# Performance work log

Hardware: AMD Instinct MI355X
Metric: run time of the kernel (lower is better)

The kernel has to match this reference:

```python
import jax, jax.numpy as jnp
import numpy as np


def setup_inputs() -> dict:
    key = jax.random.key(0)
    k1, k2, k3 = jax.random.split(key, 3)
    S, G, B, C, P = 3, 8, 2048, 512, 64
    node_feats = jax.random.normal(k1, (S, G * B, C), dtype=jnp.float32)
    weight = jax.random.normal(k2, (P, C), dtype=jnp.float32)
    smooth_factor = jax.random.normal(k3, (P,), dtype=jnp.float32)
    return {
        "node_feats": node_feats,
        "weight": weight,
        "smooth_factor": smooth_factor,
        "batch_size": B,
        "num_graphs": G,
    }


def reference(node_feats, weight, smooth_factor, batch_size, num_graphs):
    # node_feats: [S, N_scale, C] (scales stacked; torch version takes a list and cats)
    S, Ns, C = node_feats.shape
    P = weight.shape[0]
    x = node_feats.reshape(-1, C)                       # [N, C], N = S*Ns

    # RBF-style score: (2*c.x - |x|^2 - |c|^2), clamped at 0, scaled by beta
    cx = x @ weight.T                                   # [N, P]
    x_sq = jnp.sum(x * x, axis=1, keepdims=True)        # [N, 1]
    c_sq = jnp.sum(weight * weight, axis=1)[None, :]    # [1, P]
    beta = jax.nn.sigmoid(smooth_factor)                # [P]
    logits = jnp.minimum(2.0 * cx - x_sq - c_sq, 0.0) / beta[None, :]
    assign = jax.nn.softmax(logits, axis=1)             # [N, P]

    # Per-graph weighted sum (uniform batch_list), accumulated across scales:
    # out[g] = sum_{s,n in graph g} assign[s,g,n]^T feats[s,g,n]
    a = assign.reshape(S, num_graphs, batch_size, P)
    f = node_feats.reshape(S, num_graphs, batch_size, C)
    outputs = jnp.einsum('sgnp,sgnc->gpc', a, f)        # [G, P, C]
    return outputs, assign
```

## Files before the change

kernel.cpp:

```cpp
#include <hip/hip_runtime.h>
#include <math.h>

#define S_ 3
#define G_ 8
#define B_ 2048
#define C_ 512
#define P_ 64
#define N_ (S_ * G_ * B_)

typedef __attribute__((ext_vector_type(8))) short short8;
typedef __attribute__((ext_vector_type(4))) float f32x4;
typedef __attribute__((ext_vector_type(4))) unsigned int uint4v;

__device__ __forceinline__ unsigned f2bf1(float f) {
    union { float f; unsigned u; } c; c.f = f;
    unsigned u = c.u;
    u += 0x7fffu + ((u >> 16) & 1u);
    return u >> 16;
}
__device__ __forceinline__ unsigned pk2(float a, float b) {
    return f2bf1(a) | (f2bf1(b) << 16);
}
__device__ __forceinline__ void gl_lds16(const void* g, void* l) {
    __builtin_amdgcn_global_load_lds(
        (const __attribute__((address_space(1))) void*)g,
        (__attribute__((address_space(3))) void*)l, 16, 0, 0);
}
#define WAIT6_BARRIER() asm volatile("s_waitcnt vmcnt(6)\n\ts_barrier" ::: "memory")
#define WAIT0_BARRIER() asm volatile("s_waitcnt vmcnt(0)\n\ts_barrier" ::: "memory")
#define RAW_BARRIER()   asm volatile("s_barrier" ::: "memory")

__global__ __launch_bounds__(64) void prep_kernel(
    const float* __restrict__ w, const float* __restrict__ sf,
    unsigned short* __restrict__ wb, float* __restrict__ csq,
    float* __restrict__ rbeta)
{
    const int p = blockIdx.x, l = threadIdx.x;
    const float* wr = w + (size_t)p * C_ + l * 8;
    f32x4 a = *(const f32x4*)wr;
    f32x4 b = *(const f32x4*)(wr + 4);
    float s = a[0]*a[0] + a[1]*a[1] + a[2]*a[2] + a[3]*a[3]
            + b[0]*b[0] + b[1]*b[1] + b[2]*b[2] + b[3]*b[3];
    uint4v pk;
    pk.x = pk2(a[0], a[1]); pk.y = pk2(a[2], a[3]);
    pk.z = pk2(b[0], b[1]); pk.w = pk2(b[2], b[3]);
    *(uint4v*)&wb[(size_t)p * C_ + l * 8] = pk;
#pragma unroll
    for (int off = 1; off < 64; off <<= 1) s += __shfl_xor(s, off, 64);
    if (l == 0) csq[p] = s;
    if (p == 0) rbeta[l] = 1.0f + expf(-sf[l]);
}

__global__ __launch_bounds__(256, 3) void assign_v7(
    const float* __restrict__ x, const unsigned short* __restrict__ wb,
    const float* __restrict__ csq, const float* __restrict__ rbeta,
    float* __restrict__ assign, unsigned short* __restrict__ a_t)
{
    __shared__ __align__(16) float xsb[2][64 * 64];
    __shared__ __align__(16) unsigned short wsb[2][64 * 64];
    __shared__ float xsq_s[64];
    float* lg = &xsb[0][0];

    const int t = threadIdx.x, lane = t & 63, wv = t >> 6;
    const int q = lane >> 4, col = lane & 15;
    const int n0 = blockIdx.x * 64;

    const float* gx[4];
#pragma unroll
    for (int i = 0; i < 4; ++i) {
        const int row = 16 * wv + 4 * i + (lane >> 4);
        const int pr  = ((row >> 1) & 7) | (row & 8);
        gx[i] = x + (size_t)(n0 + row) * C_ + (((lane & 15) ^ pr) << 2);
    }
    const unsigned short* gw[2];
#pragma unroll
    for (int i = 0; i < 2; ++i) {
        const int p = 16 * wv + 8 * i + (lane >> 3);
        gw[i] = wb + (size_t)p * C_ + (((lane & 7) ^ (p & 7)) * 8);
    }
    const int prA = ((col >> 1) & 7) | (col & 8);
    const int wg  = col & 7;

    float csqv[4], rbv[4];
#pragma unroll
    for (int nt = 0; nt < 4; ++nt) {
        csqv[nt] = csq[16 * nt + col];
        rbv[nt]  = rbeta[16 * nt + col];
    }

    f32x4 acc[4];
#pragma unroll
    for (int nt = 0; nt < 4; ++nt) acc[nt] = (f32x4){0.f, 0.f, 0.f, 0.f};
    float xsq = 0.f;

#pragma unroll
    for (int i = 0; i < 4; ++i) gl_lds16(gx[i], &xsb[0][(16 * wv + 4 * i) * 64]);
#pragma unroll
    for (int i = 0; i < 2; ++i) gl_lds16(gw[i], &wsb[0][(16 * wv + 8 * i) * 64]);

#pragma unroll
    for (int ch = 0; ch < 8; ++ch) {
        const int cur = ch & 1;
        if (ch < 7) {
            const int k0 = (ch + 1) * 64;
#pragma unroll
            for (int i = 0; i < 4; ++i)
                gl_lds16(gx[i] + k0, &xsb[cur ^ 1][(16 * wv + 4 * i) * 64]);
#pragma unroll
            for (int i = 0; i < 2; ++i)
                gl_lds16(gw[i] + k0, &wsb[cur ^ 1][(16 * wv + 8 * i) * 64]);
            WAIT6_BARRIER();
        } else {
            WAIT0_BARRIER();
        }
#pragma unroll
        for (int s = 0; s < 2; ++s) {
            const int g0 = 8 * s + 2 * q;
            f32x4 f0 = *(const f32x4*)&xsb[cur][(16 * wv + col) * 64 + ((g0 ^ prA) << 2)];
            f32x4 f1 = *(const f32x4*)&xsb[cur][(16 * wv + col) * 64 + (((g0 + 1) ^ prA) << 2)];
            xsq += f0.x*f0.x + f0.y*f0.y + f0.z*f0.z + f0.w*f0.w
                 + f1.x*f1.x + f1.y*f1.y + f1.z*f1.z + f1.w*f1.w;
            union { uint4v u; short8 s8; } cv;
            cv.u.x = pk2(f0.x, f0.y); cv.u.y = pk2(f0.z, f0.w);
            cv.u.z = pk2(f1.x, f1.y); cv.u.w = pk2(f1.z, f1.w);
            const int wgr = 4 * s + q;
#pragma unroll
            for (int nt = 0; nt < 4; ++nt) {
                short8 bf = *(const short8*)&wsb[cur][(16 * nt + col) * 64 + ((wgr ^ wg) * 8)];
                acc[nt] = __builtin_amdgcn_mfma_f32_16x16x32_bf16(cv.s8, bf, acc[nt], 0, 0, 0);
            }
        }
        RAW_BARRIER();
    }

    xsq += __shfl_xor(xsq, 16, 64);
    xsq += __shfl_xor(xsq, 32, 64);
    if (q == 0) xsq_s[16 * wv + col] = xsq;
    __syncthreads();

    float vals[4][4];
#pragma unroll
    for (int reg = 0; reg < 4; ++reg) {
        const int row = 16 * wv + 4 * q + reg;
        const float xq = xsq_s[row];
        float vmax = -3.4e38f;
#pragma unroll
        for (int nt = 0; nt < 4; ++nt) {
            float v = 2.0f * acc[nt][reg] - xq - csqv[nt];
            v = fminf(v, 0.0f) * rbv[nt];
            vals[reg][nt] = v;
            vmax = fmaxf(vmax, v);
        }
#pragma unroll
        for (int off = 1; off < 16; off <<= 1)
            vmax = fmaxf(vmax, __shfl_xor(vmax, off, 64));
        float ss = 0.f;
#pragma unroll
        for (int nt = 0; nt < 4; ++nt) { vals[reg][nt] = __expf(vals[reg][nt] - vmax); ss += vals[reg][nt]; }
#pragma unroll
        for (int off = 1; off < 16; off <<= 1)
            ss += __shfl_xor(ss, off, 64);
        const float inv = 1.0f / ss;
#pragma unroll
        for (int nt = 0; nt < 4; ++nt) vals[reg][nt] *= inv;
    }

#pragma unroll
    for (int reg = 0; reg < 4; ++reg) {
        const int row = 16 * wv + 4 * q + reg;
#pragma unroll
        for (int nt = 0; nt < 4; ++nt)
            lg[row * 68 + 16 * nt + col] = vals[reg][nt];
    }
    __syncthreads();

#pragma unroll
    for (int i = 0; i < 4; ++i) {
        const int f = i * 256 + t;
        const int row = f >> 4, sp = (f & 15) * 4;
        *(f32x4*)(assign + (size_t)(n0 + row) * P_ + sp) = *(const f32x4*)&lg[row * 68 + sp];
    }

    const int p = lane;
    float v[16];
#pragma unroll
    for (int i = 0; i < 16; ++i) v[i] = lg[(wv * 16 + i) * 68 + p];
    uint4v d0, d1;
    d0.x = pk2(v[0], v[1]);   d0.y = pk2(v[2], v[3]);
    d0.z = pk2(v[4], v[5]);   d0.w = pk2(v[6], v[7]);
    d1.x = pk2(v[8], v[9]);   d1.y = pk2(v[10], v[11]);
    d1.z = pk2(v[12], v[13]); d1.w = pk2(v[14], v[15]);
    unsigned short* dst = a_t + (size_t)p * N_ + n0 + wv * 16;
    *(uint4v*)dst = d0;
    *(uint4v*)(dst + 8) = d1;
}

__global__ __launch_bounds__(256, 3) void group_v7(
    const float* __restrict__ x, const unsigned short* __restrict__ a_t,
    float* __restrict__ part)
{
    __shared__ __align__(16) float xsb[2][64 * 64];
    __shared__ __align__(16) unsigned short asb[2][64 * 64];

    const int t = threadIdx.x, lane = t & 63, wv = t >> 6;
    const int q = lane >> 4, col = lane & 15;
    const int g = blockIdx.x, ct = blockIdx.y, ks = blockIdx.z;
    const int c0 = ct * 64, sc = ks >> 2, b0 = (ks & 3) * 512;
    const size_t base = (size_t)sc * (G_ * B_) + (size_t)g * B_ + b0;

    const float* gx[4];
#pragma unroll
    for (int i = 0; i < 4; ++i) {
        const int n  = 16 * wv + 4 * i + (lane >> 4);
        const int pm = ((n >> 3) & 3) | (((n >> 3) & 1) << 2);
        gx[i] = x + (base + n) * C_ + c0 + (((lane & 15) ^ pm) << 2);
    }
    const unsigned short* ga[2];
#pragma unroll
    for (int i = 0; i < 2; ++i) {
        const int p = 16 * wv + 8 * i + (lane >> 3);
        ga[i] = a_t + (size_t)p * N_ + base + (((lane & 7) ^ (p & 7)) * 8);
    }
    const int cl = 16 * wv + col;
    const int permq = q | ((q & 1) << 2);
    const int cswz  = (((cl >> 2) ^ permq) << 2) | (cl & 3);
    const int ag    = col & 7;

    f32x4 acc[4];
#pragma unroll
    for (int mt = 0; mt < 4; ++mt) acc[mt] = (f32x4){0.f, 0.f, 0.f, 0.f};

#pragma unroll
    for (int i = 0; i < 4; ++i) gl_lds16(gx[i], &xsb[0][(16 * wv + 4 * i) * 64]);
#pragma unroll
    for (int i = 0; i < 2; ++i) gl_lds16(ga[i], &asb[0][(16 * wv + 8 * i) * 64]);

#pragma unroll
    for (int ch = 0; ch < 8; ++ch) {
        const int cur = ch & 1;
        if (ch < 7) {
            const int nb = (ch + 1) * 64;
#pragma unroll
            for (int i = 0; i < 4; ++i)
                gl_lds16(gx[i] + (size_t)nb * C_, &xsb[cur ^ 1][(16 * wv + 4 * i) * 64]);
#pragma unroll
            for (int i = 0; i < 2; ++i)
                gl_lds16(ga[i] + nb, &asb[cur ^ 1][(16 * wv + 8 * i) * 64]);
            WAIT6_BARRIER();
        } else {
            WAIT0_BARRIER();
        }
#pragma unroll
        for (int s = 0; s < 2; ++s) {
            const int koff = s * 32 + q * 8;
            float gv[8];
#pragma unroll
            for (int j = 0; j < 8; ++j) gv[j] = xsb[cur][(koff + j) * 64 + cswz];
            union { uint4v u; short8 s8; } cv;
            cv.u.x = pk2(gv[0], gv[1]); cv.u.y = pk2(gv[2], gv[3]);
            cv.u.z = pk2(gv[4], gv[5]); cv.u.w = pk2(gv[6], gv[7]);
            const int agr = 4 * s + q;
#pragma unroll
            for (int mt = 0; mt < 4; ++mt) {
                short8 af = *(const short8*)&asb[cur][(16 * mt + col) * 64 + ((agr ^ ag) * 8)];
                acc[mt] = __builtin_amdgcn_mfma_f32_16x16x32_bf16(af, cv.s8, acc[mt], 0, 0, 0);
            }
        }
        RAW_BARRIER();
    }

    float* pt = part + (((size_t)(g * 8 + ct) * 12) + ks) * 4096;
#pragma unroll
    for (int mt = 0; mt < 4; ++mt)
#pragma unroll
        for (int reg = 0; reg < 4; ++reg) {
            const int p = 16 * mt + 4 * q + reg;
            pt[p * 64 + cl] = acc[mt][reg];
        }
}

__global__ __launch_bounds__(256) void reduce_out(
    const float* __restrict__ part, float* __restrict__ out)
{
    const int idx = blockIdx.x * 256 + threadIdx.x;
    const int g = idx >> 15, r = idx & 32767;
    const int p = r >> 9,  c = r & 511;
    const int ct = c >> 6, cl = c & 63;
    const float* src = part + (((size_t)(g * 8 + ct) * 12)) * 4096 + p * 64 + cl;
    float s = 0.f;
#pragma unroll
    for (int ks = 0; ks < 12; ++ks) s += src[(size_t)ks * 4096];
    out[idx] = s;
}

extern "C" void kernel_launch(void* const* d_in, const int* in_sizes, int n_in,
                              void* d_out, int out_size, void* d_ws, size_t ws_size,
                              hipStream_t stream) {
    const float* x  = (const float*)d_in[0];
    const float* w  = (const float*)d_in[1];
    const float* sf = (const float*)d_in[2];

    float* out    = (float*)d_out;
    float* assign = out + (size_t)G_ * P_ * C_;

    unsigned short* wb    = (unsigned short*)d_ws;
    float*          csq   = (float*)((char*)d_ws + 65536);
    float*          rbeta = (float*)((char*)d_ws + 65792);
    unsigned short* a_t   = (unsigned short*)((char*)d_ws + 66048);
    float*          part  = (float*)((char*)d_ws + 6553600);

    prep_kernel<<<P_, 64, 0, stream>>>(w, sf, wb, csq, rbeta);
    assign_v7<<<N_ / 64, 256, 0, stream>>>(x, wb, csq, rbeta, assign, a_t);
    dim3 gridB(G_, C_ / 64, 12);
    group_v7<<<gridB, 256, 0, stream>>>(x, a_t, part);
    reduce_out<<<(G_ * P_ * C_) / 256, 256, 0, stream>>>(part, out);
}
```

Baseline: 185.9 us.

## Replace partial-sum reduce kernel with atomic accumulation and halve K-split

Removes the separate reduce_out kernel and its partial buffer. Output zeroing moves into the prep kernel, and the group kernel atomically adds its tile into the final output. The K-split drops from 12 to 6 blocks per tile, so each block processes 1024 nodes over 16 chunks, which reduces atomic contention and launch count. The trade-off is fewer blocks, 384 versus 768, which lowers parallelism, plus atomic traffic and a summation order that is no longer deterministic.

```diff
diff --git a/kernel.cpp b/kernel.cpp
--- a/kernel.cpp
+++ b/kernel.cpp
@@ -30,12 +30,17 @@
 #define WAIT0_BARRIER() asm volatile("s_waitcnt vmcnt(0)\n\ts_barrier" ::: "memory")
 #define RAW_BARRIER()   asm volatile("s_barrier" ::: "memory")
 
-__global__ __launch_bounds__(64) void prep_kernel(
+__global__ __launch_bounds__(64) void prep2_kernel(
     const float* __restrict__ w, const float* __restrict__ sf,
     unsigned short* __restrict__ wb, float* __restrict__ csq,
-    float* __restrict__ rbeta)
+    float* __restrict__ rbeta, float* __restrict__ out)
 {
     const int p = blockIdx.x, l = threadIdx.x;
+
+    f32x4* oz = (f32x4*)(out + (size_t)p * 4096);
+#pragma unroll
+    for (int i = 0; i < 16; ++i) oz[i * 64 + l] = (f32x4){0.f, 0.f, 0.f, 0.f};
+
     const float* wr = w + (size_t)p * C_ + l * 8;
     f32x4 a = *(const f32x4*)wr;
     f32x4 b = *(const f32x4*)(wr + 4);
@@ -51,7 +56,7 @@
     if (p == 0) rbeta[l] = 1.0f + expf(-sf[l]);
 }
 
-__global__ __launch_bounds__(256, 3) void assign_v7(
+__global__ __launch_bounds__(256, 3) void assign_v8(
     const float* __restrict__ x, const unsigned short* __restrict__ wb,
     const float* __restrict__ csq, const float* __restrict__ rbeta,
     float* __restrict__ assign, unsigned short* __restrict__ a_t)
@@ -195,17 +200,18 @@
     *(uint4v*)(dst + 8) = d1;
 }
 
-__global__ __launch_bounds__(256, 3) void group_v7(
+__global__ __launch_bounds__(256, 3) void group_v8(
     const float* __restrict__ x, const unsigned short* __restrict__ a_t,
-    float* __restrict__ part)
+    float* __restrict__ out)
 {
     __shared__ __align__(16) float xsb[2][64 * 64];
     __shared__ __align__(16) unsigned short asb[2][64 * 64];
 
     const int t = threadIdx.x, lane = t & 63, wv = t >> 6;
     const int q = lane >> 4, col = lane & 15;
-    const int g = blockIdx.x, ct = blockIdx.y, ks = blockIdx.z;
-    const int c0 = ct * 64, sc = ks >> 2, b0 = (ks & 3) * 512;
+    const int g = blockIdx.x, ct = blockIdx.y, ws = blockIdx.z;
+    const int c0 = ct * 64;
+    const int sc = ws >> 1, b0 = (ws & 1) * 1024;
     const size_t base = (size_t)sc * (G_ * B_) + (size_t)g * B_ + b0;
 
     const float* gx[4];
@@ -235,10 +241,10 @@
 #pragma unroll
     for (int i = 0; i < 2; ++i) gl_lds16(ga[i], &asb[0][(16 * wv + 8 * i) * 64]);
 
-#pragma unroll
-    for (int ch = 0; ch < 8; ++ch) {
+#pragma unroll 2
+    for (int ch = 0; ch < 16; ++ch) {
         const int cur = ch & 1;
-        if (ch < 7) {
+        if (ch < 15) {
             const int nb = (ch + 1) * 64;
 #pragma unroll
             for (int i = 0; i < 4; ++i)
@@ -269,28 +275,14 @@
         RAW_BARRIER();
     }
 
-    float* pt = part + (((size_t)(g * 8 + ct) * 12) + ks) * 4096;
+    float* og = out + (size_t)g * (P_ * C_);
 #pragma unroll
     for (int mt = 0; mt < 4; ++mt)
 #pragma unroll
         for (int reg = 0; reg < 4; ++reg) {
             const int p = 16 * mt + 4 * q + reg;
-            pt[p * 64 + cl] = acc[mt][reg];
-        }
-}
-
-__global__ __launch_bounds__(256) void reduce_out(
-    const float* __restrict__ part, float* __restrict__ out)
-{
-    const int idx = blockIdx.x * 256 + threadIdx.x;
-    const int g = idx >> 15, r = idx & 32767;
-    const int p = r >> 9,  c = r & 511;
-    const int ct = c >> 6, cl = c & 63;
-    const float* src = part + (((size_t)(g * 8 + ct) * 12)) * 4096 + p * 64 + cl;
-    float s = 0.f;
-#pragma unroll
-    for (int ks = 0; ks < 12; ++ks) s += src[(size_t)ks * 4096];
-    out[idx] = s;
+            atomicAdd(&og[p * C_ + c0 + cl], acc[mt][reg]);
+        }
 }
 
 extern "C" void kernel_launch(void* const* d_in, const int* in_sizes, int n_in,
@@ -307,11 +299,9 @@
     float*          csq   = (float*)((char*)d_ws + 65536);
     float*          rbeta = (float*)((char*)d_ws + 65792);
     unsigned short* a_t   = (unsigned short*)((char*)d_ws + 66048);
-    float*          part  = (float*)((char*)d_ws + 6553600);
-
-    prep_kernel<<<P_, 64, 0, stream>>>(w, sf, wb, csq, rbeta);
-    assign_v7<<<N_ / 64, 256, 0, stream>>>(x, wb, csq, rbeta, assign, a_t);
-    dim3 gridB(G_, C_ / 64, 12);
-    group_v7<<<gridB, 256, 0, stream>>>(x, a_t, part);
-    reduce_out<<<(G_ * P_ * C_) / 256, 256, 0, stream>>>(part, out);
-}
+
+    prep2_kernel<<<P_, 64, 0, stream>>>(w, sf, wb, csq, rbeta, out);
+    assign_v8<<<N_ / 64, 256, 0, stream>>>(x, wb, csq, rbeta, assign, a_t);
+    dim3 gridB(G_, C_ / 64, 6);
+    group_v8<<<gridB, 256, 0, stream>>>(x, a_t, out);
+}
```

Measured after the change: 183.1 us. About the same (-1.5%).
